# Optimization experiments

Measured on AMD Instinct MI355X. Metric: run time of the kernel, lower is better.

Reference implementation:

```python
import jax, jax.numpy as jnp
import numpy as np

RADIUS = 0.2
K = 32       # nsample
S = 1024     # npoint
BN_EPS = 1e-5


def fps(xyz, s):
    # xyz: [B, N, 3] -> indices [B, s] (farthest point sampling, start at index 0)
    B, N, _ = xyz.shape

    def step(carry, _):
        dist, last = carry                                  # [B,N], [B]
        lp = jnp.take_along_axis(xyz, last[:, None, None], axis=1)  # [B,1,3]
        d = jnp.sum((xyz - lp) ** 2, axis=-1)               # [B,N]
        dist = jnp.minimum(dist, d)
        nxt = jnp.argmax(dist, axis=-1).astype(jnp.int32)
        return (dist, nxt), last

    init = (jnp.full((B, N), jnp.inf, xyz.dtype), jnp.zeros((B,), jnp.int32))
    _, idxs = jax.lax.scan(step, init, None, length=s)      # [s, B]
    return idxs.T                                           # [B, s]


def query_ball(new_xyz, xyz, radius, k):
    # new_xyz: [B,S,3], xyz: [B,N,3] -> first k in-ball indices [B,S,k]
    B, N, _ = xyz.shape
    d2 = jnp.sum((new_xyz[:, :, None, :] - xyz[:, None, :, :]) ** 2, axis=-1)  # [B,S,N]
    cand = jnp.where(d2 <= radius * radius, jnp.arange(N, dtype=jnp.int32)[None, None, :], N)
    idx = jnp.sort(cand, axis=-1)[..., :k]                  # first-k by index, pytorch3d order
    first = idx[..., :1]
    idx = jnp.where(idx == N, first, idx)                   # replicate first valid index
    return jnp.minimum(idx, N - 1)


def gather_pts(pts, idx):
    # pts: [B,N,C], idx: [B,S,K] -> [B,S,K,C]
    B, N, C = pts.shape
    _, s, k = idx.shape
    g = jnp.take_along_axis(pts, idx.reshape(B, s * k, 1), axis=1)
    return g.reshape(B, s, k, C)


def conv_bn_relu(x, W, b, g, be):
    # x: [B,S,K,Cin], W: [Cout,Cin] (1x1 conv), training-mode BatchNorm over (B,S,K)
    y = jnp.einsum('bskc,oc->bsko', x, W) + b
    mu = jnp.mean(y, axis=(0, 1, 2))
    var = jnp.var(y, axis=(0, 1, 2))
    y = (y - mu) * jax.lax.rsqrt(var + BN_EPS) * g + be
    return jax.nn.relu(y)


def setup_inputs() -> dict:
    key = jax.random.key(0)
    ks = jax.random.split(key, 8)
    B, N, D = 8, 8192, 64
    inp = {
        'xyz': jax.random.uniform(ks[0], (B, 3, N), dtype=jnp.float32),
        'points': jax.random.normal(ks[1], (B, D, N), dtype=jnp.float32),
    }
    dims = [(64, 67), (64, 64), (128, 64)]
    for i, (o, c) in enumerate(dims):
        inp[f'W{i}'] = jax.random.normal(ks[2 + i], (o, c), dtype=jnp.float32) * 0.05
        inp[f'b{i}'] = jnp.zeros((o,), jnp.float32)
        inp[f'g{i}'] = jnp.ones((o,), jnp.float32)
        inp[f'be{i}'] = jnp.zeros((o,), jnp.float32)
    return inp


def reference(xyz, points, W0, b0, g0, be0, W1, b1, g1, be1, W2, b2, g2, be2):
    # xyz: [B,3,N], points: [B,D,N]
    xyz_n = jnp.transpose(xyz, (0, 2, 1))                   # [B,N,3]
    pts_n = jnp.transpose(points, (0, 2, 1))                # [B,N,D]
    idx = fps(xyz_n, S)                                     # [B,S]
    new_xyz = jnp.take_along_axis(xyz_n, idx[..., None], axis=1)  # [B,S,3]
    gidx = query_ball(new_xyz, xyz_n, RADIUS, K)            # [B,S,K]
    gxyz = (gather_pts(xyz_n, gidx) - new_xyz[:, :, None, :]) / RADIUS  # [B,S,K,3]
    gpts = gather_pts(pts_n, gidx)                          # [B,S,K,D]
    feat = jnp.concatenate([gpts, gxyz], axis=-1)           # [B,S,K,D+3]
    feat = conv_bn_relu(feat, W0, b0, g0, be0)
    feat = conv_bn_relu(feat, W1, b1, g1, be1)
    feat = conv_bn_relu(feat, W2, b2, g2, be2)
    new_points = jnp.max(feat, axis=2)                      # [B,S,Cout]
    return (jnp.transpose(new_xyz, (0, 2, 1)), jnp.transpose(new_points, (0, 2, 1)))
```

## Files before the change

kernel.cpp:

```cpp
#include <hip/hip_runtime.h>

#define BB 8
#define NN 8192
#define SS 1024
#define KK 32
#define NPIX (BB*SS*KK)
#define R2C 0.04f
#define EPS 1e-5f

#define FT 1024
#define FW (FT/64)
#define PPT (NN/FT)
#define NCELL 4096

#define OFF_IDX      0u
#define OFF_NEWXYZ   (OFF_IDX + BB*SS*4)
#define OFF_GIDX     (OFF_NEWXYZ + BB*SS*3*4)
#define OFF_XYZN     (OFF_GIDX + BB*SS*KK*4)
#define OFF_PTSN     (OFF_XYZN + BB*NN*3*4)
#define OFF_Y0       (OFF_PTSN + BB*NN*64*4)
#define OFF_Y1       (OFF_Y0 + NPIX*64*2)
#define OFF_MAXMIN   (OFF_Y1 + NPIX*64*2)
#define OFF_P0       (OFF_MAXMIN + BB*SS*128*2*4)
#define OFF_P1       (OFF_P0 + 1024*128*4)
#define OFF_P2       (OFF_P1 + 1024*128*4)
#define OFF_SC       (OFF_P2 + 1024*256*4)

__device__ __forceinline__ unsigned short f2bf(float x){
    unsigned u = __float_as_uint(x);
    unsigned r = (u + 0x7FFFu + ((u >> 16) & 1u)) >> 16;
    return (unsigned short)r;
}
__device__ __forceinline__ float bf2f(unsigned h){
    return __uint_as_float(h << 16);
}
__device__ __forceinline__ float sqdist3(float dx, float dy, float dz){
    return __fadd_rn(__fadd_rn(__fmul_rn(dx,dx), __fmul_rn(dy,dy)), __fmul_rn(dz,dz));
}
__device__ __forceinline__ int spread4(int v){
    return (v&1) | ((v&2)<<2) | ((v&4)<<4) | ((v&8)<<6);
}

template<int CTRL>
__device__ __forceinline__ unsigned long long dpp_max_step(unsigned long long k){
    int lo = (int)(unsigned)k;
    int hi = (int)(unsigned)(k >> 32);
    int olo = __builtin_amdgcn_update_dpp(0, lo, CTRL, 0xf, 0xf, true);
    int ohi = __builtin_amdgcn_update_dpp(0, hi, CTRL, 0xf, 0xf, true);
    unsigned long long o = ((unsigned long long)(unsigned)ohi << 32) | (unsigned)olo;
    return (o > k) ? o : k;
}
__device__ __forceinline__ unsigned long long wave_max_u64(unsigned long long k){
    k = dpp_max_step<0x111>(k);
    k = dpp_max_step<0x112>(k);
    k = dpp_max_step<0x114>(k);
    k = dpp_max_step<0x118>(k);
    k = dpp_max_step<0x142>(k);
    k = dpp_max_step<0x143>(k);
    return k;
}

__global__ __launch_bounds__(256) void t_kernel(const float* __restrict__ xyz,
                                                const float* __restrict__ pts,
                                                float* __restrict__ xyz_n,
                                                float* __restrict__ pts_n){
    int gid = blockIdx.x * 256 + threadIdx.x;
    int b = gid >> 13, i = gid & (NN - 1);
    const float* xb = xyz + (size_t)b * 3 * NN;
    float x = xb[i], y = xb[NN + i], z = xb[2 * NN + i];
    float* xd = xyz_n + ((size_t)b * NN + i) * 3;
    xd[0] = x; xd[1] = y; xd[2] = z;
    const float* pb = pts + (size_t)b * 64 * NN + i;
    float4* pd = (float4*)(pts_n + ((size_t)b * NN + i) * 64);
#pragma unroll
    for (int q = 0; q < 16; ++q){
        float4 v;
        v.x = pb[(q*4+0)*NN]; v.y = pb[(q*4+1)*NN];
        v.z = pb[(q*4+2)*NN]; v.w = pb[(q*4+3)*NN];
        pd[q] = v;
    }
}

__global__ __launch_bounds__(FT) void fps_kernel(const float* __restrict__ xyz,
                                                 float* __restrict__ newxyz,
                                                 float* __restrict__ out){
    __shared__ float sx[NN], sy[NN], sz[NN];
    __shared__ int   si[NN];
    __shared__ int   hist[NCELL];
    __shared__ int   waveTot[FW];
    __shared__ unsigned long long cells[4];
    int b = blockIdx.x, tid = threadIdx.x;
    int wave = tid >> 6, lane = tid & 63;
    const float* xb = xyz + (size_t)b * 3 * NN;

    int cell[PPT];
#pragma unroll
    for (int j = 0; j < PPT; ++j){
        int i = tid + j * FT;
        float x = xb[i], y = xb[NN + i], z = xb[2*NN + i];
        sx[i] = x; sy[i] = y; sz[i] = z;
        int cx = min(15, max(0, (int)(x * 16.f)));
        int cy = min(15, max(0, (int)(y * 16.f)));
        int cz = min(15, max(0, (int)(z * 16.f)));
        cell[j] = spread4(cx) | (spread4(cy) << 1) | (spread4(cz) << 2);
    }
#pragma unroll
    for (int k = 0; k < NCELL/FT; ++k) hist[tid * (NCELL/FT) + k] = 0;
    if (tid < 4) cells[tid] = 0ull;
    __syncthreads();
#pragma unroll
    for (int j = 0; j < PPT; ++j) atomicAdd(&hist[cell[j]], 1);
    __syncthreads();
    {
        int base0 = tid * (NCELL/FT);
        int sum4 = 0;
#pragma unroll
        for (int k = 0; k < NCELL/FT; ++k) sum4 += hist[base0 + k];
        int s = sum4;
#pragma unroll
        for (int m = 1; m < 64; m <<= 1){
            int v = __shfl_up(s, m);
            if (lane >= m) s += v;
        }
        if (lane == 63) waveTot[wave] = s;
        __syncthreads();
        int wbase = 0;
#pragma unroll
        for (int w2 = 0; w2 < FW; ++w2) if (w2 < wave) wbase += waveTot[w2];
        int run = wbase + s - sum4;
#pragma unroll
        for (int k = 0; k < NCELL/FT; ++k){
            int h = hist[base0 + k];
            hist[base0 + k] = run;
            run += h;
        }
    }
    __syncthreads();
#pragma unroll
    for (int j = 0; j < PPT; ++j){
        int pos = atomicAdd(&hist[cell[j]], 1);
        si[pos] = tid + j * FT;
    }
    __syncthreads();
    float px[PPT], py[PPT], pz[PPT], dist[PPT];
    int oi[PPT];
    float bxmin =  1e30f, bxmax = -1e30f;
    float bymin =  1e30f, bymax = -1e30f;
    float bzmin =  1e30f, bzmax = -1e30f;
#pragma unroll
    for (int j = 0; j < PPT; ++j){
        int g = si[tid * PPT + j];
        oi[j] = g;
        float x = sx[g], y = sy[g], z = sz[g];
        px[j] = x; py[j] = y; pz[j] = z;
        bxmin = fminf(bxmin, x); bxmax = fmaxf(bxmax, x);
        bymin = fminf(bymin, y); bymax = fmaxf(bymax, y);
        bzmin = fminf(bzmin, z); bzmax = fmaxf(bzmax, z);
        dist[j] = __int_as_float(0x7f800000);
    }
    __syncthreads();

    unsigned long long mykey = 0ull;
    unsigned long long lane63cache = 0ull;
    float tmax = __int_as_float(0x7f800000);
    int w = 0;
    for (int t = 0; t < SS; ++t){
        if (tid == 0) hist[t] = w;
        float lx = sx[w], ly = sy[w], lz = sz[w];
        float cdx = __fsub_rn(lx, fminf(fmaxf(lx, bxmin), bxmax));
        float cdy = __fsub_rn(ly, fminf(fmaxf(ly, bymin), bymax));
        float cdz = __fsub_rn(lz, fminf(fmaxf(lz, bzmin), bzmax));
        float d_bb = sqdist3(cdx, cdy, cdz);
        bool active = d_bb < tmax;
        unsigned long long bal = __ballot(active);
        if (active){
            {
#pragma clang fp contract(off)
#pragma unroll
                for (int j = 0; j < PPT; ++j){
                    float dx = px[j] - lx;
                    float dy = py[j] - ly;
                    float dz = pz[j] - lz;
                    float d = ((dx*dx) + (dy*dy)) + (dz*dz);
                    dist[j] = fminf(dist[j], d);
                }
            }
            float m0 = fmaxf(dist[0], dist[1]);
            float m1 = fmaxf(dist[2], dist[3]);
            float m2 = fmaxf(dist[4], dist[5]);
            float m3 = fmaxf(dist[6], dist[7]);
            m0 = fmaxf(m0, m1); m2 = fmaxf(m2, m3);
            float maxd = fmaxf(m0, m2);
            int bo = 0x7fffffff;
#pragma unroll
            for (int j = 0; j < PPT; ++j)
                if (dist[j] == maxd) bo = min(bo, oi[j]);
            mykey = ((unsigned long long)__float_as_uint(maxd) << 32)
                  | (unsigned)(~bo);
            tmax = maxd;
        }
        if (bal){
            unsigned long long k = wave_max_u64(mykey);
            if (lane == 63) lane63cache = k;
        }
        if (lane == 63) atomicMax(&cells[t & 3], lane63cache);
        if (tid == 0) cells[(t + 2) & 3] = 0ull;
        __syncthreads();
        unsigned long long km = cells[t & 3];
        w = (int)(~(unsigned)km);
    }
    __syncthreads();
    for (int t2 = tid; t2 < SS; t2 += FT){
        int hw = hist[t2];
        float x = sx[hw], y = sy[hw], z = sz[hw];
        out[(size_t)b * 3 * SS + t2]          = x;
        out[(size_t)b * 3 * SS + SS + t2]     = y;
        out[(size_t)b * 3 * SS + 2*SS + t2]   = z;
        float* nw = newxyz + ((size_t)b * SS + t2) * 3;
        nw[0] = x; nw[1] = y; nw[2] = z;
    }
}

__global__ __launch_bounds__(256) void qb_kernel(const float* __restrict__ xyz,
                                                 const float* __restrict__ newxyz,
                                                 int* __restrict__ gidx){
    int wid = (blockIdx.x * 256 + threadIdx.x) >> 6;
    int lane = threadIdx.x & 63;
    int b = wid >> 10;
    const float* nw = newxyz + (size_t)wid * 3;
    float cx = nw[0], cy = nw[1], cz = nw[2];
    const float* xb = xyz + (size_t)b * 3 * NN;
    int total = 0, firstIdx = -1;
    int* gout = gidx + (size_t)wid * KK;
    for (int base = 0; base < NN; base += 64){
        int i = base + lane;
        float dx = __fsub_rn(cx, xb[i]);
        float dy = __fsub_rn(cy, xb[NN + i]);
        float dz = __fsub_rn(cz, xb[2*NN + i]);
        float d2 = sqdist3(dx, dy, dz);
        bool in = (d2 <= R2C);
        unsigned long long m = __ballot(in);
        int pos = total + __popcll(m & ((1ull << lane) - 1ull));
        if (in && pos < KK) gout[pos] = i;
        if (firstIdx < 0 && m) firstIdx = base + (__ffsll((unsigned long long)m) - 1);
        total += __popcll(m);
        if (total >= KK) break;
    }
    if (total < KK){
        int f = (total > 0) ? firstIdx : (NN - 1);
        for (int p = total + lane; p < KK; p += 64) gout[p] = f;
    }
}

__global__ __launch_bounds__(256) void l0_kernel(const float* __restrict__ pts_n,
                                                 const float* __restrict__ xyz_n,
                                                 const float* __restrict__ newxyz,
                                                 const int* __restrict__ gidx,
                                                 const float* __restrict__ W0,
                                                 const float* __restrict__ b0,
                                                 uint4* __restrict__ y0,
                                                 float* __restrict__ part0){
    __shared__ float lsum[4][64][2];
    int tid = threadIdx.x;
    int pixel = blockIdx.x * 256 + tid;
    int sample = pixel >> 5;
    int b = sample >> 10;
    int gi = gidx[pixel];
    int wave = tid >> 6, lane = tid & 63;

    float ff[67];
    const float4* prow = (const float4*)(pts_n + ((size_t)b * NN + gi) * 64);
#pragma unroll
    for (int q = 0; q < 16; ++q){
        float4 v = prow[q];
        ff[q*4] = v.x; ff[q*4+1] = v.y; ff[q*4+2] = v.z; ff[q*4+3] = v.w;
    }
    const float* pr = xyz_n + ((size_t)b * NN + gi) * 3;
    const float* nw = newxyz + (size_t)sample * 3;
    ff[64] = __fsub_rn(pr[0], nw[0]) / 0.2f;
    ff[65] = __fsub_rn(pr[1], nw[1]) / 0.2f;
    ff[66] = __fsub_rn(pr[2], nw[2]) / 0.2f;

    for (int oc = 0; oc < 8; ++oc){
        float acc[8];
#pragma unroll
        for (int j = 0; j < 8; ++j) acc[j] = b0[oc*8+j];
#pragma unroll
        for (int c = 0; c < 67; ++c){
            float fe = ff[c];
#pragma unroll
            for (int j = 0; j < 8; ++j) acc[j] += fe * W0[(oc*8+j)*67 + c];
        }
        uint4 pk;
        unsigned us[8];
#pragma unroll
        for (int j = 0; j < 8; ++j){
            float v = acc[j];
            float s1 = v, s2 = v * v;
#pragma unroll
            for (int m = 1; m <= 32; m <<= 1){
                s1 += __shfl_xor(s1, m);
                s2 += __shfl_xor(s2, m);
            }
            if (lane == 0){ lsum[wave][oc*8+j][0] = s1; lsum[wave][oc*8+j][1] = s2; }
            us[j] = f2bf(v);
        }
        pk.x = us[0] | (us[1] << 16);
        pk.y = us[2] | (us[3] << 16);
        pk.z = us[4] | (us[5] << 16);
        pk.w = us[6] | (us[7] << 16);
        y0[(size_t)pixel * 8 + oc] = pk;
    }
    __syncthreads();
    if (tid < 128){
        float s = lsum[0][tid>>1][tid&1] + lsum[1][tid>>1][tid&1]
                + lsum[2][tid>>1][tid&1] + lsum[3][tid>>1][tid&1];
        part0[(size_t)blockIdx.x * 128 + tid] = s;
    }
}

__global__ __launch_bounds__(256) void l1_kernel(const uint4* __restrict__ y0,
                                                 const float* __restrict__ scale0,
                                                 const float* __restrict__ shift0,
                                                 const float* __restrict__ W1,
                                                 const float* __restrict__ b1,
                                                 uint4* __restrict__ y1,
                                                 float* __restrict__ part1){
    __shared__ float lsum[4][64][2];
    int tid = threadIdx.x;
    int pixel = blockIdx.x * 256 + tid;
    int wave = tid >> 6, lane = tid & 63;

    float x[64];
#pragma unroll
    for (int q = 0; q < 8; ++q){
        uint4 v = y0[(size_t)pixel * 8 + q];
        unsigned w[4] = {v.x, v.y, v.z, v.w};
#pragma unroll
        for (int r = 0; r < 4; ++r){
            int c = q*8 + r*2;
            x[c]   = fmaxf(bf2f(w[r] & 0xFFFFu) * scale0[c]   + shift0[c],   0.f);
            x[c+1] = fmaxf(bf2f(w[r] >> 16)     * scale0[c+1] + shift0[c+1], 0.f);
        }
    }
    for (int oc = 0; oc < 8; ++oc){
        float acc[8];
#pragma unroll
        for (int j = 0; j < 8; ++j) acc[j] = b1[oc*8+j];
#pragma unroll
        for (int c = 0; c < 64; ++c){
            float fe = x[c];
#pragma unroll
            for (int j = 0; j < 8; ++j) acc[j] += fe * W1[(oc*8+j)*64 + c];
        }
        uint4 pk;
        unsigned us[8];
#pragma unroll
        for (int j = 0; j < 8; ++j){
            float v = acc[j];
            float s1 = v, s2 = v * v;
#pragma unroll
            for (int m = 1; m <= 32; m <<= 1){
                s1 += __shfl_xor(s1, m);
                s2 += __shfl_xor(s2, m);
            }
            if (lane == 0){ lsum[wave][oc*8+j][0] = s1; lsum[wave][oc*8+j][1] = s2; }
            us[j] = f2bf(v);
        }
        pk.x = us[0] | (us[1] << 16);
        pk.y = us[2] | (us[3] << 16);
        pk.z = us[4] | (us[5] << 16);
        pk.w = us[6] | (us[7] << 16);
        y1[(size_t)pixel * 8 + oc] = pk;
    }
    __syncthreads();
    if (tid < 128){
        float s = lsum[0][tid>>1][tid&1] + lsum[1][tid>>1][tid&1]
                + lsum[2][tid>>1][tid&1] + lsum[3][tid>>1][tid&1];
        part1[(size_t)blockIdx.x * 128 + tid] = s;
    }
}

__global__ __launch_bounds__(256) void l2_kernel(const uint4* __restrict__ y1,
                                                 const float* __restrict__ scale1,
                                                 const float* __restrict__ shift1,
                                                 const float* __restrict__ W2,
                                                 const float* __restrict__ b2,
                                                 float* __restrict__ maxmin,
                                                 float* __restrict__ part2){
    __shared__ float lsum[4][128][2];
    int tid = threadIdx.x;
    int pixel = blockIdx.x * 256 + tid;
    int sample = pixel >> 5;
    int wave = tid >> 6, lane = tid & 63;

    float x[64];
#pragma unroll
    for (int q = 0; q < 8; ++q){
        uint4 v = y1[(size_t)pixel * 8 + q];
        unsigned w[4] = {v.x, v.y, v.z, v.w};
#pragma unroll
        for (int r = 0; r < 4; ++r){
            int c = q*8 + r*2;
            x[c]   = fmaxf(bf2f(w[r] & 0xFFFFu) * scale1[c]   + shift1[c],   0.f);
            x[c+1] = fmaxf(bf2f(w[r] >> 16)     * scale1[c+1] + shift1[c+1], 0.f);
        }
    }
    for (int oc = 0; oc < 16; ++oc){
        float acc[8];
#pragma unroll
        for (int j = 0; j < 8; ++j) acc[j] = b2[oc*8+j];
#pragma unroll
        for (int c = 0; c < 64; ++c){
            float fe = x[c];
#pragma unroll
            for (int j = 0; j < 8; ++j) acc[j] += fe * W2[(oc*8+j)*64 + c];
        }
#pragma unroll
        for (int j = 0; j < 8; ++j){
            float v = acc[j];
            int ch = oc*8 + j;
            float mx = v, mn = v;
#pragma unroll
            for (int m = 1; m <= 16; m <<= 1){
                mx = fmaxf(mx, __shfl_xor(mx, m));
                mn = fminf(mn, __shfl_xor(mn, m));
            }
            float s1 = v, s2 = v * v;
#pragma unroll
            for (int m = 1; m <= 32; m <<= 1){
                s1 += __shfl_xor(s1, m);
                s2 += __shfl_xor(s2, m);
            }
            if (lane == 0){ lsum[wave][ch][0] = s1; lsum[wave][ch][1] = s2; }
            if ((tid & 31) == 0){
                float* mm = maxmin + ((size_t)sample * 128 + ch) * 2;
                mm[0] = mx; mm[1] = mn;
            }
        }
    }
    __syncthreads();
    {
        float s = lsum[0][tid>>1][tid&1] + lsum[1][tid>>1][tid&1]
                + lsum[2][tid>>1][tid&1] + lsum[3][tid>>1][tid&1];
        part2[(size_t)blockIdx.x * 256 + tid] = s;
    }
}

__global__ __launch_bounds__(1024) void fin_kernel(const float* __restrict__ part, int O,
                           const float* __restrict__ g, const float* __restrict__ be,
                           float* __restrict__ scale, float* __restrict__ shift){
    __shared__ float ls[1024];
    __shared__ float tot[256];
    int tid = threadIdx.x;
    int M = 2 * O;
    int C = 1024 / M;
    int m = tid & (M - 1);
    int chunk = tid / M;
    int per = 1024 / C;
    float s = 0.f;
    for (int r = 0; r < per; ++r){
        int blk = chunk * per + r;
        s += part[(size_t)blk * M + m];
    }
    ls[tid] = s;
    __syncthreads();
    if (tid < M){
        float tt = 0.f;
        for (int c2 = 0; c2 < C; ++c2) tt += ls[c2 * M + tid];
        tot[tid] = tt;
    }
    __syncthreads();
    if (tid < O){
        float s1 = tot[2*tid], s2 = tot[2*tid+1];
        float inv = 1.0f / (float)NPIX;
        float mu = s1 * inv;
        float var = s2 * inv - mu * mu;
        float rs = 1.0f / sqrtf(var + EPS);
        float sc = rs * g[tid];
        scale[tid] = sc;
        shift[tid] = be[tid] - mu * sc;
    }
}

__global__ __launch_bounds__(256) void out_kernel(const float* __restrict__ maxmin,
                                                  const float* __restrict__ scale2,
                                                  const float* __restrict__ shift2,
                                                  float* __restrict__ out){
    int gid = blockIdx.x * 256 + threadIdx.x;
    int s = gid & 1023;
    int o = (gid >> 10) & 127;
    int b = gid >> 17;
    int sample = b * 1024 + s;
    float2 mm = ((const float2*)maxmin)[(size_t)sample * 128 + o];
    float sc = scale2[o], sh = shift2[o];
    float v = (sc >= 0.f) ? mm.x : mm.y;
    out[gid] = fmaxf(v * sc + sh, 0.f);
}

extern "C" void kernel_launch(void* const* d_in, const int* in_sizes, int n_in,
                              void* d_out, int out_size, void* d_ws, size_t ws_size,
                              hipStream_t stream) {
    const float* xyz = (const float*)d_in[0];
    const float* pts = (const float*)d_in[1];
    const float* W0 = (const float*)d_in[2];
    const float* b0 = (const float*)d_in[3];
    const float* g0 = (const float*)d_in[4];
    const float* be0 = (const float*)d_in[5];
    const float* W1 = (const float*)d_in[6];
    const float* b1 = (const float*)d_in[7];
    const float* g1 = (const float*)d_in[8];
    const float* be1 = (const float*)d_in[9];
    const float* W2 = (const float*)d_in[10];
    const float* b2 = (const float*)d_in[11];
    const float* g2 = (const float*)d_in[12];
    const float* be2 = (const float*)d_in[13];

    char* ws = (char*)d_ws;
    float* newxyz = (float*)(ws + OFF_NEWXYZ);
    int*   gidx   = (int*)(ws + OFF_GIDX);
    float* xyz_n  = (float*)(ws + OFF_XYZN);
    float* pts_n  = (float*)(ws + OFF_PTSN);
    uint4* y0     = (uint4*)(ws + OFF_Y0);
    uint4* y1     = (uint4*)(ws + OFF_Y1);
    float* maxmin = (float*)(ws + OFF_MAXMIN);
    float* part0  = (float*)(ws + OFF_P0);
    float* part1  = (float*)(ws + OFF_P1);
    float* part2  = (float*)(ws + OFF_P2);
    float* sc     = (float*)(ws + OFF_SC);
    float* scale0 = sc,        *shift0 = sc + 64;
    float* scale1 = sc + 128,  *shift1 = sc + 192;
    float* scale2 = sc + 256,  *shift2 = sc + 384;

    float* out = (float*)d_out;
    float* out_np = out + BB * 3 * SS;

    hipLaunchKernelGGL(t_kernel, dim3(256), dim3(256), 0, stream, xyz, pts, xyz_n, pts_n);
    hipLaunchKernelGGL(fps_kernel, dim3(BB), dim3(FT), 0, stream, xyz, newxyz, out);
    hipLaunchKernelGGL(qb_kernel, dim3(2048), dim3(256), 0, stream, xyz, newxyz, gidx);
    hipLaunchKernelGGL(l0_kernel, dim3(1024), dim3(256), 0, stream,
                       pts_n, xyz_n, newxyz, gidx, W0, b0, y0, part0);
    hipLaunchKernelGGL(fin_kernel, dim3(1), dim3(1024), 0, stream, part0, 64, g0, be0, scale0, shift0);
    hipLaunchKernelGGL(l1_kernel, dim3(1024), dim3(256), 0, stream,
                       y0, scale0, shift0, W1, b1, y1, part1);
    hipLaunchKernelGGL(fin_kernel, dim3(1), dim3(1024), 0, stream, part1, 64, g1, be1, scale1, shift1);
    hipLaunchKernelGGL(l2_kernel, dim3(1024), dim3(256), 0, stream,
                       y1, scale1, shift1, W2, b2, maxmin, part2);
    hipLaunchKernelGGL(fin_kernel, dim3(1), dim3(1024), 0, stream, part2, 128, g2, be2, scale2, shift2);
    hipLaunchKernelGGL(out_kernel, dim3(4096), dim3(256), 0, stream, maxmin, scale2, shift2, out_np);
}
```

Baseline: 1.375 ms.

## Fold transpose into FPS launch, use per-step FPS slots, vectorize BN finalize

The separate transpose kernel is merged into the FPS launch as extra blocks, so the transpose runs on otherwise idle CUs while the 8 serial FPS blocks execute, and one launch is removed. The FPS argmax exchange now uses a dedicated shared slot per step (1024 u64) instead of a 4-slot ring with clearing, dropping one store per iteration at the cost of 8KB more LDS. The BN finalize kernel reads partial sums as float4 and reduces in a single pass. Risk: the extra transpose blocks now need the FPS kernel's large LDS footprint, which may limit how many co-reside.

```diff
diff --git a/kernel.cpp b/kernel.cpp
--- a/kernel.cpp
+++ b/kernel.cpp
@@ -12,6 +12,7 @@
 #define FW (FT/64)
 #define PPT (NN/FT)
 #define NCELL 4096
+#define TBLK 64
 
 #define OFF_IDX      0u
 #define OFF_NEWXYZ   (OFF_IDX + BB*SS*4)
@@ -60,36 +61,39 @@
     return k;
 }
 
-__global__ __launch_bounds__(256) void t_kernel(const float* __restrict__ xyz,
-                                                const float* __restrict__ pts,
-                                                float* __restrict__ xyz_n,
-                                                float* __restrict__ pts_n){
-    int gid = blockIdx.x * 256 + threadIdx.x;
-    int b = gid >> 13, i = gid & (NN - 1);
-    const float* xb = xyz + (size_t)b * 3 * NN;
-    float x = xb[i], y = xb[NN + i], z = xb[2 * NN + i];
-    float* xd = xyz_n + ((size_t)b * NN + i) * 3;
-    xd[0] = x; xd[1] = y; xd[2] = z;
-    const float* pb = pts + (size_t)b * 64 * NN + i;
-    float4* pd = (float4*)(pts_n + ((size_t)b * NN + i) * 64);
-#pragma unroll
-    for (int q = 0; q < 16; ++q){
-        float4 v;
-        v.x = pb[(q*4+0)*NN]; v.y = pb[(q*4+1)*NN];
-        v.z = pb[(q*4+2)*NN]; v.w = pb[(q*4+3)*NN];
-        pd[q] = v;
-    }
-}
-
 __global__ __launch_bounds__(FT) void fps_kernel(const float* __restrict__ xyz,
+                                                 const float* __restrict__ pts,
                                                  float* __restrict__ newxyz,
-                                                 float* __restrict__ out){
+                                                 float* __restrict__ out,
+                                                 float* __restrict__ xyz_n,
+                                                 float* __restrict__ pts_n){
     __shared__ float sx[NN], sy[NN], sz[NN];
     __shared__ int   si[NN];
     __shared__ int   hist[NCELL];
     __shared__ int   waveTot[FW];
-    __shared__ unsigned long long cells[4];
-    int b = blockIdx.x, tid = threadIdx.x;
+    __shared__ unsigned long long cells[SS];
+    int tid = threadIdx.x;
+
+    if (blockIdx.x >= 8){
+        int gid = (blockIdx.x - 8) * FT + tid;
+        int b = gid >> 13, i = gid & (NN - 1);
+        const float* xb = xyz + (size_t)b * 3 * NN;
+        float x = xb[i], y = xb[NN + i], z = xb[2 * NN + i];
+        float* xd = xyz_n + ((size_t)b * NN + i) * 3;
+        xd[0] = x; xd[1] = y; xd[2] = z;
+        const float* pb = pts + (size_t)b * 64 * NN + i;
+        float4* pd = (float4*)(pts_n + ((size_t)b * NN + i) * 64);
+#pragma unroll
+        for (int q = 0; q < 16; ++q){
+            float4 v;
+            v.x = pb[(q*4+0)*NN]; v.y = pb[(q*4+1)*NN];
+            v.z = pb[(q*4+2)*NN]; v.w = pb[(q*4+3)*NN];
+            pd[q] = v;
+        }
+        return;
+    }
+
+    int b = blockIdx.x;
     int wave = tid >> 6, lane = tid & 63;
     const float* xb = xyz + (size_t)b * 3 * NN;
 
@@ -106,7 +110,7 @@
     }
 #pragma unroll
     for (int k = 0; k < NCELL/FT; ++k) hist[tid * (NCELL/FT) + k] = 0;
-    if (tid < 4) cells[tid] = 0ull;
+    cells[tid] = 0ull;
     __syncthreads();
 #pragma unroll
     for (int j = 0; j < PPT; ++j) atomicAdd(&hist[cell[j]], 1);
@@ -203,10 +207,9 @@
             unsigned long long k = wave_max_u64(mykey);
             if (lane == 63) lane63cache = k;
         }
-        if (lane == 63) atomicMax(&cells[t & 3], lane63cache);
-        if (tid == 0) cells[(t + 2) & 3] = 0ull;
+        if (lane == 63) atomicMax(&cells[t], lane63cache);
         __syncthreads();
-        unsigned long long km = cells[t & 3];
+        unsigned long long km = cells[t];
         w = (int)(~(unsigned)km);
     }
     __syncthreads();
@@ -450,36 +453,39 @@
 __global__ __launch_bounds__(1024) void fin_kernel(const float* __restrict__ part, int O,
                            const float* __restrict__ g, const float* __restrict__ be,
                            float* __restrict__ scale, float* __restrict__ shift){
-    __shared__ float ls[1024];
-    __shared__ float tot[256];
+    __shared__ float4 ls[1024];
     int tid = threadIdx.x;
     int M = 2 * O;
-    int C = 1024 / M;
-    int m = tid & (M - 1);
-    int chunk = tid / M;
-    int per = 1024 / C;
-    float s = 0.f;
+    int V = M >> 2;
+    int NC = 1024 / V;
+    int q = tid & (V - 1);
+    int c = tid / V;
+    int per = 1024 / NC;
+    const float4* p4 = (const float4*)part;
+    float4 s = {0.f, 0.f, 0.f, 0.f};
     for (int r = 0; r < per; ++r){
-        int blk = chunk * per + r;
-        s += part[(size_t)blk * M + m];
-    }
-    ls[tid] = s;
-    __syncthreads();
-    if (tid < M){
-        float tt = 0.f;
-        for (int c2 = 0; c2 < C; ++c2) tt += ls[c2 * M + tid];
-        tot[tid] = tt;
-    }
-    __syncthreads();
-    if (tid < O){
-        float s1 = tot[2*tid], s2 = tot[2*tid+1];
+        int blk = c * per + r;
+        float4 v = p4[(size_t)blk * V + q];
+        s.x += v.x; s.y += v.y; s.z += v.z; s.w += v.w;
+    }
+    ls[c * V + q] = s;
+    __syncthreads();
+    if (tid < V){
+        float4 t4 = ls[tid];
+        for (int c2 = 1; c2 < NC; ++c2){
+            float4 v = ls[c2 * V + tid];
+            t4.x += v.x; t4.y += v.y; t4.z += v.z; t4.w += v.w;
+        }
         float inv = 1.0f / (float)NPIX;
-        float mu = s1 * inv;
-        float var = s2 * inv - mu * mu;
-        float rs = 1.0f / sqrtf(var + EPS);
-        float sc = rs * g[tid];
-        scale[tid] = sc;
-        shift[tid] = be[tid] - mu * sc;
+        int ch0 = 2 * tid, ch1 = 2 * tid + 1;
+        float mu0 = t4.x * inv;
+        float var0 = t4.y * inv - mu0 * mu0;
+        float sc0 = (1.0f / sqrtf(var0 + EPS)) * g[ch0];
+        scale[ch0] = sc0; shift[ch0] = be[ch0] - mu0 * sc0;
+        float mu1 = t4.z * inv;
+        float var1 = t4.w * inv - mu1 * mu1;
+        float sc1 = (1.0f / sqrtf(var1 + EPS)) * g[ch1];
+        scale[ch1] = sc1; shift[ch1] = be[ch1] - mu1 * sc1;
     }
 }
 
@@ -535,8 +541,8 @@
     float* out = (float*)d_out;
     float* out_np = out + BB * 3 * SS;
 
-    hipLaunchKernelGGL(t_kernel, dim3(256), dim3(256), 0, stream, xyz, pts, xyz_n, pts_n);
-    hipLaunchKernelGGL(fps_kernel, dim3(BB), dim3(FT), 0, stream, xyz, newxyz, out);
+    hipLaunchKernelGGL(fps_kernel, dim3(8 + TBLK), dim3(FT), 0, stream,
+                       xyz, pts, newxyz, out, xyz_n, pts_n);
     hipLaunchKernelGGL(qb_kernel, dim3(2048), dim3(256), 0, stream, xyz, newxyz, gidx);
     hipLaunchKernelGGL(l0_kernel, dim3(1024), dim3(256), 0, stream,
                        pts_n, xyz_n, newxyz, gidx, W0, b0, y0, part0);
```

Measured after the change: 1.241 ms. -9.7%, faster.
